# Kernel tuning notes

Hardware: AMD Instinct MI355X
Metric: run time of the kernel (lower is better)

Reference implementation:

```python
import jax, jax.numpy as jnp
import numpy as np


def gcn_conv(x, src, dst, W, b, num_nodes):
    # PyG GCNConv with add_self_loops=True, symmetric normalization.
    # src/dst already include self-loops.
    ones = jnp.ones(src.shape[0], dtype=x.dtype)
    deg = jax.ops.segment_sum(ones, dst, num_segments=num_nodes)  # [N]
    dinv = jnp.where(deg > 0, jax.lax.rsqrt(deg), 0.0)
    norm = dinv[src] * dinv[dst]                                   # [E+N]
    h = x @ W                                                      # [N, out]
    msg = h[src] * norm[:, None]                                   # gather + scale
    out = jax.ops.segment_sum(msg, dst, num_segments=num_nodes)    # scatter-add
    return out + b


def setup_inputs() -> dict:
    key = jax.random.key(0)
    k1, k2, k3, k4 = jax.random.split(key, 4)
    N, E = 50000, 1600000
    IN, HID, OUT = 1536, 256, 128
    x = jax.random.normal(k1, (N, IN), dtype=jnp.float32)
    edge_index = jax.random.randint(k2, (2, E), 0, N, dtype=jnp.int64)
    # Glorot-style scaled weights
    W1 = jax.random.normal(k3, (IN, HID), dtype=jnp.float32) / np.sqrt(IN)
    W2 = jax.random.normal(k4, (HID, OUT), dtype=jnp.float32) / np.sqrt(HID)
    b1 = jnp.zeros((HID,), dtype=jnp.float32)
    b2 = jnp.zeros((OUT,), dtype=jnp.float32)
    return {"x": x, "edge_index": edge_index, "W1": W1, "b1": b1,
            "W2": W2, "b2": b2, "num_nodes": N}


def reference(x, edge_index, W1, b1, W2, b2, num_nodes):
    loop = jnp.arange(num_nodes, dtype=edge_index.dtype)
    src = jnp.concatenate([edge_index[0], loop])
    dst = jnp.concatenate([edge_index[1], loop])
    h = gcn_conv(x, src, dst, W1, b1, num_nodes)
    h = jax.nn.relu(h)
    h = gcn_conv(h, src, dst, W2, b2, num_nodes)
    # F.normalize(h, dim=1): x / max(||x||_2, 1e-12)
    nrm = jnp.linalg.norm(h, axis=1, keepdims=True)
    return h / jnp.maximum(nrm, 1e-12)
```

## Files before the change

kernel.cpp:

```cpp
#include <hip/hip_runtime.h>

typedef __attribute__((ext_vector_type(4))) float f32x4;
typedef __attribute__((ext_vector_type(2))) float f32x2;
typedef __attribute__((ext_vector_type(8))) short s16x8;

static __device__ __forceinline__ unsigned short f2bf(float f) {
  unsigned int u = __builtin_bit_cast(unsigned int, f);
  u += 0x7fffu + ((u >> 16) & 1u);
  return (unsigned short)(u >> 16);
}
static __device__ __forceinline__ float bf2f(unsigned short h) {
  unsigned int u = ((unsigned int)h) << 16;
  return __builtin_bit_cast(float, u);
}

static __device__ __forceinline__ void gload_lds16(const void* g, void* l) {
  __builtin_amdgcn_global_load_lds(
      (const __attribute__((address_space(1))) unsigned int*)g,
      (__attribute__((address_space(3))) unsigned int*)l, 16, 0, 0);
}

__global__ void zero_k(int* p, int n) {
  int i = blockIdx.x * 256 + threadIdx.x;
  if (i < n) p[i] = 0;
}
__global__ void deg_count_k(const int* __restrict__ edges, int* cnt, int E) {
  int e = blockIdx.x * 256 + threadIdx.x;
  if (e < E) atomicAdd(&cnt[edges[E + e]], 1);
}

__global__ __launch_bounds__(256) void scan1_k(const int* __restrict__ cnt,
                                               int* __restrict__ loc,
                                               int* __restrict__ bsum, int N) {
  int t = threadIdx.x;
  int i0 = blockIdx.x * 1024 + t * 4;
  int c[4];
#pragma unroll
  for (int j = 0; j < 4; ++j) c[j] = (i0 + j < N) ? cnt[i0 + j] : 0;
  int tsum = c[0] + c[1] + c[2] + c[3];
  int lane = t & 63, wv = t >> 6;
  int incl = tsum;
#pragma unroll
  for (int off = 1; off < 64; off <<= 1) {
    int u = __shfl_up(incl, off, 64);
    if (lane >= off) incl += u;
  }
  __shared__ int ws[4];
  if (lane == 63) ws[wv] = incl;
  __syncthreads();
  int wbase = 0;
  for (int w = 0; w < wv; ++w) wbase += ws[w];
  int run = wbase + incl - tsum;
#pragma unroll
  for (int j = 0; j < 4; ++j) {
    if (i0 + j < N) loc[i0 + j] = run;
    run += c[j];
  }
  if (t == 255) bsum[blockIdx.x] = wbase + incl;
}
__global__ void scan2_k(int* bsum, int nb) {
  int lane = threadIdx.x;
  int v = (lane < nb) ? bsum[lane] : 0;
  int incl = v;
#pragma unroll
  for (int off = 1; off < 64; off <<= 1) {
    int u = __shfl_up(incl, off, 64);
    if (lane >= off) incl += u;
  }
  if (lane < nb) bsum[lane] = incl - v;
}
__global__ void addoff_k(int* loc, int* cursor, const int* __restrict__ bsum,
                         const int* __restrict__ cnt, float* __restrict__ dinv, int N) {
  int i = blockIdx.x * 256 + threadIdx.x;
  if (i < N) {
    int v = loc[i] + bsum[i >> 10];
    loc[i] = v;
    cursor[i] = v;
    dinv[i] = rsqrtf((float)(cnt[i] + 1));
  }
}
__global__ void fill_k(const int* __restrict__ edges, int* cursor,
                       int* __restrict__ csr, int E) {
  int e = blockIdx.x * 256 + threadIdx.x;
  if (e < E) {
    int s = edges[e], d = edges[E + e];
    int pos = atomicAdd(&cursor[d], 1);
    csr[pos] = s;
  }
}

__global__ __launch_bounds__(256) void convw_k(const float* __restrict__ W,
                                               unsigned short* __restrict__ Wt,
                                               int K, int Nn) {
  __shared__ float t[32][33];
  const int tx = threadIdx.x & 31, ty = threadIdx.x >> 5;
  const int k0 = blockIdx.x * 32, n0 = blockIdx.y * 32;
#pragma unroll
  for (int r = 0; r < 32; r += 8)
    t[r + ty][tx] = W[(long long)(k0 + r + ty) * Nn + (n0 + tx)];
  __syncthreads();
#pragma unroll
  for (int r = 0; r < 32; r += 8)
    Wt[(long long)(n0 + r + ty) * K + (k0 + tx)] = f2bf(t[tx][r + ty]);
}

template <int KTOT, int NTOT, int BM, bool A_BF16>
__global__ __launch_bounds__(256, 3) void gemm_k(
    const void* __restrict__ Aptr, const unsigned short* __restrict__ Bt,
    const float* __restrict__ dinv, unsigned short* __restrict__ outg, int M) {
  constexpr int BK = 32;
  constexpr int LDA = BK + 8;
  constexpr int MI = BM / 16;
  constexpr int STRIP = NTOT / 4;
  constexpr int NF = STRIP / 16;
  constexpr int BCH = (NTOT / 16) / 4;
  constexpr int ACH = (BM / 16) / 4;
  constexpr int NT = KTOT / BK;
  constexpr int TPR = 256 / BM;
  constexpr int FPT = BK / TPR;

  __shared__ unsigned short Asm_[2][BM * LDA];
  __shared__ unsigned short Bsm_[2][NTOT * BK];

  const int tid = threadIdx.x;
  const int wave = tid >> 6;
  const int lane = tid & 63;
  const int fr = lane & 15;
  const int quad = lane >> 4;
  const int m0 = blockIdx.x * BM;

  f32x4 acc[MI][NF];
#pragma unroll
  for (int i = 0; i < MI; ++i)
#pragma unroll
    for (int j = 0; j < NF; ++j) { f32x4 z = {0.f, 0.f, 0.f, 0.f}; acc[i][j] = z; }

  const int sl_r = lane >> 2;
  const int sl_s = (lane & 3) ^ ((lane >> 3) & 3);

  auto stageB = [&](int k0, int buf) {
#pragma unroll
    for (int c = 0; c < BCH; ++c) {
      int cc = wave * BCH + c;
      int r = cc * 16 + sl_r;
      const unsigned short* gp = Bt + (long long)r * KTOT + k0 + sl_s * 8;
      gload_lds16(gp, &Bsm_[buf][cc * 512]);
    }
  };
  auto stageA_h = [&](int k0, int buf) {
    const unsigned short* Ah = (const unsigned short*)Aptr;
#pragma unroll
    for (int c = 0; c < ACH; ++c) {
      int cc = wave * ACH + c;
      int r = cc * 16 + sl_r;
      const unsigned short* gp = Ah + (long long)(m0 + r) * KTOT + k0 + sl_s * 8;
      gload_lds16(gp, &Asm_[buf][cc * 512]);
    }
  };

  const int sr = tid / TPR;
  const int sc = (tid % TPR) * FPT;
  const bool arow_ok = (m0 + sr) < M;
  const float* arowf = (const float*)Aptr + (long long)(m0 + sr) * KTOT;
  float va[FPT];
  auto loadA = [&](int k0) {
    if (arow_ok) {
#pragma unroll
      for (int c = 0; c < FPT / 4; ++c) {
        f32x4 v = *(const f32x4*)(arowf + k0 + sc + c * 4);
#pragma unroll
        for (int j = 0; j < 4; ++j) va[c * 4 + j] = v[j];
      }
    } else {
#pragma unroll
      for (int j = 0; j < FPT; ++j) va[j] = 0.0f;
    }
  };
  auto cvtWriteA = [&](int buf) {
#pragma unroll
    for (int c = 0; c < FPT / 8; ++c) {
      s16x8 h;
#pragma unroll
      for (int j = 0; j < 8; ++j) h[j] = (short)f2bf(va[c * 8 + j]);
      *(s16x8*)&Asm_[buf][sr * LDA + sc + c * 8] = h;
    }
  };

  stageB(0, 0);
  if constexpr (A_BF16) {
    stageA_h(0, 0);
  } else {
    loadA(0);
    cvtWriteA(0);
    if (NT > 1) loadA(BK);
  }

  const int xsl = (fr >> 1) & 3;
  for (int kt = 0; kt < NT; ++kt) {
    const int cur = kt & 1;
    __syncthreads();
    if (kt + 1 < NT) {
      stageB((kt + 1) * BK, cur ^ 1);
      if constexpr (A_BF16) {
        stageA_h((kt + 1) * BK, cur ^ 1);
      } else {
        cvtWriteA(cur ^ 1);
        if (kt + 2 < NT) loadA((kt + 2) * BK);
      }
    }

    s16x8 af[MI], bfr[NF];
#pragma unroll
    for (int mi = 0; mi < MI; ++mi) {
      if constexpr (A_BF16)
        af[mi] = *(const s16x8*)&Asm_[cur][(mi * 16 + fr) * BK + ((quad ^ xsl) << 3)];
      else
        af[mi] = *(const s16x8*)&Asm_[cur][(mi * 16 + fr) * LDA + quad * 8];
    }
#pragma unroll
    for (int ni = 0; ni < NF; ++ni)
      bfr[ni] = *(const s16x8*)&Bsm_[cur][(wave * STRIP + ni * 16 + fr) * BK + ((quad ^ xsl) << 3)];
#pragma unroll
    for (int mi = 0; mi < MI; ++mi)
#pragma unroll
      for (int ni = 0; ni < NF; ++ni)
        acc[mi][ni] = __builtin_amdgcn_mfma_f32_16x16x32_bf16(af[mi], bfr[ni], acc[mi][ni], 0, 0, 0);
  }

#pragma unroll
  for (int mi = 0; mi < MI; ++mi) {
    int mbase = mi * 16 + quad * 4;
#pragma unroll
    for (int r = 0; r < 4; ++r) {
      int gm = m0 + mbase + r;
      if (gm < M) {
        float dv = dinv[gm];
#pragma unroll
        for (int ni = 0; ni < NF; ++ni) {
          int col = wave * STRIP + ni * 16 + fr;
          outg[(long long)gm * NTOT + col] = f2bf(acc[mi][ni][r] * dv);
        }
      }
    }
  }
}

__global__ __launch_bounds__(256) void agg1_k(const int* __restrict__ csr,
                                              const int* __restrict__ row,
                                              const int* __restrict__ cnt,
                                              const unsigned short* __restrict__ g,
                                              const float* __restrict__ bias,
                                              const float* __restrict__ dinv,
                                              unsigned short* __restrict__ h, int N) {
  const int wave = threadIdx.x >> 6, lane = threadIdx.x & 63;
  const int node = blockIdx.x * 4 + wave;
  if (node >= N) return;
  const int grp = lane >> 5, sub = lane & 31;
  const int f0 = sub * 8;
  float s[8];
#pragma unroll
  for (int k = 0; k < 8; ++k) s[k] = 0.0f;
  const int start = row[node], len = cnt[node];
  int j = 0;
  for (; j + 8 <= len; j += 8) {
    int idx[4];
#pragma unroll
    for (int t = 0; t < 4; ++t) idx[t] = csr[start + j + t * 2 + grp];
    s16x8 v[4];
#pragma unroll
    for (int t = 0; t < 4; ++t) v[t] = *(const s16x8*)&g[(long long)idx[t] * 256 + f0];
#pragma unroll
    for (int t = 0; t < 4; ++t)
#pragma unroll
      for (int k = 0; k < 8; ++k) s[k] += bf2f((unsigned short)v[t][k]);
  }
  for (; j < len; j += 2) {
    int jt = j + grp;
    bool val = jt < len;
    int idx = csr[start + (val ? jt : 0)];
    s16x8 v = *(const s16x8*)&g[(long long)idx * 256 + f0];
    float m = val ? 1.0f : 0.0f;
#pragma unroll
    for (int k = 0; k < 8; ++k) s[k] += m * bf2f((unsigned short)v[k]);
  }
#pragma unroll
  for (int k = 0; k < 8; ++k) s[k] += __shfl_xor(s[k], 32, 64);
  s16x8 sv = *(const s16x8*)&g[(long long)node * 256 + f0];
#pragma unroll
  for (int k = 0; k < 8; ++k) s[k] += bf2f((unsigned short)sv[k]);
  const float dv = dinv[node];
  f32x4 b0 = *(const f32x4*)&bias[f0];
  f32x4 b1v = *(const f32x4*)&bias[f0 + 4];
  if (grp == 0) {
    s16x8 o;
#pragma unroll
    for (int k = 0; k < 4; ++k) o[k] = (short)f2bf(fmaxf(0.0f, b0[k] + dv * s[k]));
#pragma unroll
    for (int k = 0; k < 4; ++k) o[4 + k] = (short)f2bf(fmaxf(0.0f, b1v[k] + dv * s[4 + k]));
    *(s16x8*)&h[(long long)node * 256 + f0] = o;
  }
}

__global__ __launch_bounds__(256) void agg2_k(const int* __restrict__ csr,
                                              const int* __restrict__ row,
                                              const int* __restrict__ cnt,
                                              const unsigned short* __restrict__ g,
                                              const float* __restrict__ b2,
                                              const float* __restrict__ dinv,
                                              float* __restrict__ out, int N) {
  const int wave = threadIdx.x >> 6, lane = threadIdx.x & 63;
  const int node = blockIdx.x * 4 + wave;
  if (node >= N) return;
  const int grp = lane >> 4, sub = lane & 15;
  const int f0 = sub * 8;
  float s[8];
#pragma unroll
  for (int k = 0; k < 8; ++k) s[k] = 0.0f;
  const int start = row[node], len = cnt[node];
  int j = 0;
  for (; j + 8 <= len; j += 8) {
    int idx[2];
#pragma unroll
    for (int t = 0; t < 2; ++t) idx[t] = csr[start + j + t * 4 + grp];
    s16x8 v[2];
#pragma unroll
    for (int t = 0; t < 2; ++t) v[t] = *(const s16x8*)&g[(long long)idx[t] * 128 + f0];
#pragma unroll
    for (int t = 0; t < 2; ++t)
#pragma unroll
      for (int k = 0; k < 8; ++k) s[k] += bf2f((unsigned short)v[t][k]);
  }
  for (; j < len; j += 4) {
    int jt = j + grp;
    bool val = jt < len;
    int idx = csr[start + (val ? jt : 0)];
    s16x8 v = *(const s16x8*)&g[(long long)idx * 128 + f0];
    float m = val ? 1.0f : 0.0f;
#pragma unroll
    for (int k = 0; k < 8; ++k) s[k] += m * bf2f((unsigned short)v[k]);
  }
#pragma unroll
  for (int k = 0; k < 8; ++k) s[k] += __shfl_xor(s[k], 16, 64);
#pragma unroll
  for (int k = 0; k < 8; ++k) s[k] += __shfl_xor(s[k], 32, 64);
  s16x8 sv = *(const s16x8*)&g[(long long)node * 128 + f0];
#pragma unroll
  for (int k = 0; k < 8; ++k) s[k] += bf2f((unsigned short)sv[k]);
  const float dv = dinv[node];
  f32x4 b0 = *(const f32x4*)&b2[f0];
  f32x4 b1v = *(const f32x4*)&b2[f0 + 4];
  float x[8];
#pragma unroll
  for (int k = 0; k < 4; ++k) x[k] = b0[k] + dv * s[k];
#pragma unroll
  for (int k = 0; k < 4; ++k) x[4 + k] = b1v[k] + dv * s[4 + k];
  float ss = 0.0f;
#pragma unroll
  for (int k = 0; k < 8; ++k) ss += x[k] * x[k];
#pragma unroll
  for (int off = 1; off < 16; off <<= 1) ss += __shfl_xor(ss, off, 64);
  const float inv = 1.0f / fmaxf(sqrtf(ss), 1e-12f);
  if (grp == 0) {
    f32x4 o0 = {x[0] * inv, x[1] * inv, x[2] * inv, x[3] * inv};
    f32x4 o1 = {x[4] * inv, x[5] * inv, x[6] * inv, x[7] * inv};
    *(f32x4*)&out[(long long)node * 128 + f0] = o0;
    *(f32x4*)&out[(long long)node * 128 + f0 + 4] = o1;
  }
}

extern "C" void kernel_launch(void* const* d_in, const int* in_sizes, int n_in,
                              void* d_out, int out_size, void* d_ws, size_t ws_size,
                              hipStream_t stream) {
  const float* x = (const float*)d_in[0];
  const int* edges = (const int*)d_in[1];
  const float* W1 = (const float*)d_in[2];
  const float* b1 = (const float*)d_in[3];
  const float* W2 = (const float*)d_in[4];
  const float* b2 = (const float*)d_in[5];
  float* out = (float*)d_out;

  const int HID = in_sizes[3];
  const int OUT = in_sizes[5];
  const int IN = in_sizes[2] / HID;
  const int N = in_sizes[0] / IN;
  const int E = in_sizes[1] / 2;

  size_t off = 0;
  auto carve = [&](size_t bytes) {
    void* p = (char*)d_ws + off;
    off += (bytes + 255) & ~(size_t)255;
    return p;
  };
  int* cnt = (int*)carve((size_t)N * 4);
  int* cursor = (int*)carve((size_t)N * 4);
  int* row = (int*)carve((size_t)N * 4);
  int* bsum = (int*)carve(64 * 4);
  int* csr = (int*)carve((size_t)E * 4 + 1024);
  float* dinv = (float*)carve((size_t)N * 4);
  unsigned short* W1t = (unsigned short*)carve((size_t)IN * HID * 2);
  unsigned short* W2t = (unsigned short*)carve((size_t)HID * OUT * 2);
  unsigned short* g1 = (unsigned short*)carve((size_t)N * HID * 2);
  unsigned short* acc1 = (unsigned short*)carve((size_t)N * HID * 2);
  unsigned short* g2 = (unsigned short*)carve((size_t)N * OUT * 2);
  (void)ws_size; (void)n_in; (void)out_size;

  const int nb = (N + 1023) / 1024;

  zero_k<<<(N + 255) / 256, 256, 0, stream>>>(cnt, N);
  deg_count_k<<<(E + 255) / 256, 256, 0, stream>>>(edges, cnt, E);

  scan1_k<<<nb, 256, 0, stream>>>(cnt, row, bsum, N);
  scan2_k<<<1, 64, 0, stream>>>(bsum, nb);
  addoff_k<<<(N + 255) / 256, 256, 0, stream>>>(row, cursor, bsum, cnt, dinv, N);
  fill_k<<<(E + 255) / 256, 256, 0, stream>>>(edges, cursor, csr, E);

  convw_k<<<dim3(IN / 32, HID / 32), 256, 0, stream>>>(W1, W1t, IN, HID);
  convw_k<<<dim3(HID / 32, OUT / 32), 256, 0, stream>>>(W2, W2t, HID, OUT);

  constexpr int BM = 64;
  int mtiles = (N + BM - 1) / BM;
  gemm_k<1536, 256, BM, false><<<mtiles, 256, 0, stream>>>(x, W1t, dinv, g1, N);
  agg1_k<<<(N + 3) / 4, 256, 0, stream>>>(csr, row, cnt, g1, b1, dinv, acc1, N);
  gemm_k<256, 128, BM, true><<<mtiles, 256, 0, stream>>>(acc1, W2t, dinv, g2, N);
  agg2_k<<<(N + 3) / 4, 256, 0, stream>>>(csr, row, cnt, g2, b2, dinv, out, N);
}
```

Before: 866.7 us.

## Deepen GEMM pipeline to triple-buffered LDS with 128-row tiles and register prefetch

Reworks the GEMM main loop into a three-stage LDS ring with a three-deep register prefetch of fp32 A rows. Waits use explicit s_waitcnt vmcnt counts and raw s_barrier instead of __syncthreads. The M tile grows from 64 to 128 rows, and A loads become nontemporal with clamped row indices instead of bounds branches. The goal is to hide the global-load latency of the large x matrix and halve how often B is reloaded. The cost is more LDS and registers per block (launch bounds drop to 2 blocks per SM) and fragile hand-counted wait logic.

```diff
diff --git a/kernel.cpp b/kernel.cpp
--- a/kernel.cpp
+++ b/kernel.cpp
@@ -104,11 +104,11 @@
     Wt[(long long)(n0 + r + ty) * K + (k0 + tx)] = f2bf(t[tx][r + ty]);
 }
 
-template <int KTOT, int NTOT, int BM, bool A_BF16>
-__global__ __launch_bounds__(256, 3) void gemm_k(
+template <int KTOT, int NTOT, bool A_BF16>
+__global__ __launch_bounds__(256, 2) void gemm_k(
     const void* __restrict__ Aptr, const unsigned short* __restrict__ Bt,
     const float* __restrict__ dinv, unsigned short* __restrict__ outg, int M) {
-  constexpr int BK = 32;
+  constexpr int BM = 128, BK = 32;
   constexpr int LDA = BK + 8;
   constexpr int MI = BM / 16;
   constexpr int STRIP = NTOT / 4;
@@ -118,9 +118,11 @@
   constexpr int NT = KTOT / BK;
   constexpr int TPR = 256 / BM;
   constexpr int FPT = BK / TPR;
-
-  __shared__ unsigned short Asm_[2][BM * LDA];
-  __shared__ unsigned short Bsm_[2][NTOT * BK];
+  constexpr int ASZ = A_BF16 ? (BM * BK) : (BM * LDA);
+  constexpr int VM_N = A_BF16 ? 4 : 12;
+
+  __shared__ unsigned short Asm_[3][ASZ];
+  __shared__ unsigned short Bsm_[3][NTOT * BK];
 
   const int tid = threadIdx.x;
   const int wave = tid >> 6;
@@ -160,55 +162,31 @@
 
   const int sr = tid / TPR;
   const int sc = (tid % TPR) * FPT;
-  const bool arow_ok = (m0 + sr) < M;
-  const float* arowf = (const float*)Aptr + (long long)(m0 + sr) * KTOT;
-  float va[FPT];
-  auto loadA = [&](int k0) {
-    if (arow_ok) {
-#pragma unroll
-      for (int c = 0; c < FPT / 4; ++c) {
-        f32x4 v = *(const f32x4*)(arowf + k0 + sc + c * 4);
-#pragma unroll
-        for (int j = 0; j < 4; ++j) va[c * 4 + j] = v[j];
-      }
-    } else {
-#pragma unroll
-      for (int j = 0; j < FPT; ++j) va[j] = 0.0f;
-    }
-  };
-  auto cvtWriteA = [&](int buf) {
-#pragma unroll
-    for (int c = 0; c < FPT / 8; ++c) {
-      s16x8 h;
-#pragma unroll
-      for (int j = 0; j < 8; ++j) h[j] = (short)f2bf(va[c * 8 + j]);
-      *(s16x8*)&Asm_[buf][sr * LDA + sc + c * 8] = h;
-    }
-  };
-
-  stageB(0, 0);
-  if constexpr (A_BF16) {
-    stageA_h(0, 0);
-  } else {
-    loadA(0);
-    cvtWriteA(0);
-    if (NT > 1) loadA(BK);
-  }
+  const int arow = min(m0 + sr, M - 1);
+  const float* arowf = (const float*)Aptr + (long long)arow * KTOT;
+  float va0[FPT], va1[FPT], va2[FPT];
+
+#define LOADA(VA, K0)                                                          \
+  do {                                                                         \
+    _Pragma("unroll") for (int c = 0; c < FPT / 4; ++c) {                      \
+      f32x4 v = __builtin_nontemporal_load(                                    \
+          (const f32x4*)(arowf + (K0) + sc + c * 4));                          \
+      _Pragma("unroll") for (int j = 0; j < 4; ++j) VA[c * 4 + j] = v[j];      \
+    }                                                                          \
+  } while (0)
+
+#define CVTWA(VA, BUF)                                                         \
+  do {                                                                         \
+    _Pragma("unroll") for (int c = 0; c < FPT / 8; ++c) {                      \
+      s16x8 hh;                                                                \
+      _Pragma("unroll") for (int j = 0; j < 8; ++j)                            \
+          hh[j] = (short)f2bf(VA[c * 8 + j]);                                  \
+      *(s16x8*)&Asm_[BUF][sr * LDA + sc + c * 8] = hh;                         \
+    }                                                                          \
+  } while (0)
 
   const int xsl = (fr >> 1) & 3;
-  for (int kt = 0; kt < NT; ++kt) {
-    const int cur = kt & 1;
-    __syncthreads();
-    if (kt + 1 < NT) {
-      stageB((kt + 1) * BK, cur ^ 1);
-      if constexpr (A_BF16) {
-        stageA_h((kt + 1) * BK, cur ^ 1);
-      } else {
-        cvtWriteA(cur ^ 1);
-        if (kt + 2 < NT) loadA((kt + 2) * BK);
-      }
-    }
-
+  auto compute = [&](int cur) {
     s16x8 af[MI], bfr[NF];
 #pragma unroll
     for (int mi = 0; mi < MI; ++mi) {
@@ -225,7 +203,58 @@
 #pragma unroll
       for (int ni = 0; ni < NF; ++ni)
         acc[mi][ni] = __builtin_amdgcn_mfma_f32_16x16x32_bf16(af[mi], bfr[ni], acc[mi][ni], 0, 0, 0);
-  }
+  };
+
+  if constexpr (A_BF16) {
+    stageB(0, 0); stageA_h(0, 0);
+    stageB(BK, 1); stageA_h(BK, 1);
+  } else {
+    {
+      float vt[FPT];
+      LOADA(vt, 0);  CVTWA(vt, 0);
+      LOADA(vt, BK); CVTWA(vt, 1);
+    }
+    stageB(0, 0);
+    stageB(BK, 1);
+    __builtin_amdgcn_sched_barrier(0);
+    LOADA(va0, 2 * BK);
+    LOADA(va1, 3 * BK);
+    LOADA(va2, 4 * BK);
+  }
+
+#define GITER(J, P, PS, VA)                                                    \
+  {                                                                            \
+    if constexpr (VM_N == 12)                                                  \
+      asm volatile("s_waitcnt vmcnt(12) lgkmcnt(0)" ::: "memory");             \
+    else                                                                       \
+      asm volatile("s_waitcnt vmcnt(4) lgkmcnt(0)" ::: "memory");              \
+    __builtin_amdgcn_s_barrier();                                              \
+    __builtin_amdgcn_sched_barrier(0);                                         \
+    int ks_ = ((J) + 2 < NT) ? ((J) + 2) * BK : (KTOT - BK);                   \
+    stageB(ks_, (PS));                                                         \
+    if constexpr (A_BF16) {                                                    \
+      stageA_h(ks_, (PS));                                                     \
+    } else {                                                                   \
+      __builtin_amdgcn_sched_barrier(0);   \
+      CVTWA(VA, (PS));                                                         \
+      int kl_ = ((J) + 5 < NT) ? ((J) + 5) * BK : (KTOT - BK);                 \
+      LOADA(VA, kl_);                                                          \
+    }                                                                          \
+    compute(P);                                                                \
+  }
+
+  int j = 0;
+  for (; j + 3 <= NT; j += 3) {
+    GITER(j, 0, 2, va0);
+    GITER(j + 1, 1, 0, va1);
+    GITER(j + 2, 2, 1, va2);
+  }
+  if constexpr (NT % 3 >= 1) GITER(j, 0, 2, va0);
+  if constexpr (NT % 3 == 2) GITER(j + 1, 1, 0, va1);
+
+#undef GITER
+#undef LOADA
+#undef CVTWA
 
 #pragma unroll
   for (int mi = 0; mi < MI; ++mi) {
@@ -417,10 +446,9 @@
   convw_k<<<dim3(IN / 32, HID / 32), 256, 0, stream>>>(W1, W1t, IN, HID);
   convw_k<<<dim3(HID / 32, OUT / 32), 256, 0, stream>>>(W2, W2t, HID, OUT);
 
-  constexpr int BM = 64;
-  int mtiles = (N + BM - 1) / BM;
-  gemm_k<1536, 256, BM, false><<<mtiles, 256, 0, stream>>>(x, W1t, dinv, g1, N);
+  int mtiles = (N + 127) / 128;
+  gemm_k<1536, 256, false><<<mtiles, 256, 0, stream>>>(x, W1t, dinv, g1, N);
   agg1_k<<<(N + 3) / 4, 256, 0, stream>>>(csr, row, cnt, g1, b1, dinv, acc1, N);
-  gemm_k<256, 128, BM, true><<<mtiles, 256, 0, stream>>>(acc1, W2t, dinv, g2, N);
+  gemm_k<256, 128, true><<<mtiles, 256, 0, stream>>>(acc1, W2t, dinv, g2, N);
   agg2_k<<<(N + 3) / 4, 256, 0, stream>>>(csr, row, cnt, g2, b2, dinv, out, N);
 }
```

Result: slower. 891.8 us (+2.9%).

## Drop LDS staging in GEMM; load MFMA fragments directly from global memory

Applied to the files above, without the earlier changes.

Rewrites the GEMM kernel so each wave loads its A rows and B columns straight from global memory into MFMA register fragments, double-buffered in registers, with no LDS tiles and no block barriers. Blocks grow to 512 threads covering 128 rows, and each wave owns 32 rows and half of the output columns. A is read with nontemporal loads and converted to bf16 in registers. This removes LDS traffic and synchronisation, but B is now re-read from global or L2 by every wave, and the per-lane 16-byte loads are less coalesced.

```diff
diff --git a/kernel.cpp b/kernel.cpp
--- a/kernel.cpp
+++ b/kernel.cpp
@@ -12,12 +12,6 @@
 static __device__ __forceinline__ float bf2f(unsigned short h) {
   unsigned int u = ((unsigned int)h) << 16;
   return __builtin_bit_cast(float, u);
-}
-
-static __device__ __forceinline__ void gload_lds16(const void* g, void* l) {
-  __builtin_amdgcn_global_load_lds(
-      (const __attribute__((address_space(1))) unsigned int*)g,
-      (__attribute__((address_space(3))) unsigned int*)l, 16, 0, 0);
 }
 
 __global__ void zero_k(int* p, int n) {
@@ -104,30 +98,30 @@
     Wt[(long long)(n0 + r + ty) * K + (k0 + tx)] = f2bf(t[tx][r + ty]);
 }
 
-template <int KTOT, int NTOT, int BM, bool A_BF16>
-__global__ __launch_bounds__(256, 3) void gemm_k(
+template <int KTOT, int NTOT, bool A_BF16>
+__global__ __launch_bounds__(512, 2) void gemm_k(
     const void* __restrict__ Aptr, const unsigned short* __restrict__ Bt,
     const float* __restrict__ dinv, unsigned short* __restrict__ outg, int M) {
   constexpr int BK = 32;
-  constexpr int LDA = BK + 8;
-  constexpr int MI = BM / 16;
-  constexpr int STRIP = NTOT / 4;
+  constexpr int NT = KTOT / BK;
+  constexpr int STRIP = NTOT / 2;
   constexpr int NF = STRIP / 16;
-  constexpr int BCH = (NTOT / 16) / 4;
-  constexpr int ACH = (BM / 16) / 4;
-  constexpr int NT = KTOT / BK;
-  constexpr int TPR = 256 / BM;
-  constexpr int FPT = BK / TPR;
-
-  __shared__ unsigned short Asm_[2][BM * LDA];
-  __shared__ unsigned short Bsm_[2][NTOT * BK];
+  constexpr int MI = 2;
 
   const int tid = threadIdx.x;
   const int wave = tid >> 6;
   const int lane = tid & 63;
   const int fr = lane & 15;
   const int quad = lane >> 4;
-  const int m0 = blockIdx.x * BM;
+  const int mq = wave >> 1;
+  const int nh = wave & 1;
+  const int m0 = blockIdx.x * 128 + mq * 32;
+
+  const float* Af = (const float*)Aptr;
+  const unsigned short* Ah = (const unsigned short*)Aptr;
+  long long ar0 = (long long)min(m0 + 0 * 16 + fr, M - 1) * KTOT;
+  long long ar1 = (long long)min(m0 + 1 * 16 + fr, M - 1) * KTOT;
+  const unsigned short* bbase = Bt + (long long)(nh * STRIP + fr) * KTOT;
 
   f32x4 acc[MI][NF];
 #pragma unroll
@@ -135,109 +129,81 @@
 #pragma unroll
     for (int j = 0; j < NF; ++j) { f32x4 z = {0.f, 0.f, 0.f, 0.f}; acc[i][j] = z; }
 
-  const int sl_r = lane >> 2;
-  const int sl_s = (lane & 3) ^ ((lane >> 3) & 3);
-
-  auto stageB = [&](int k0, int buf) {
-#pragma unroll
-    for (int c = 0; c < BCH; ++c) {
-      int cc = wave * BCH + c;
-      int r = cc * 16 + sl_r;
-      const unsigned short* gp = Bt + (long long)r * KTOT + k0 + sl_s * 8;
-      gload_lds16(gp, &Bsm_[buf][cc * 512]);
+  f32x4 vaA[MI][2], vaB[MI][2];
+  s16x8 ahA[MI], ahB[MI];
+  s16x8 bfA[NF], bfB[NF];
+
+#define LDA_(VA, AH, KT)                                                       \
+  do {                                                                         \
+    const int k0_ = (KT) * BK + quad * 8;                                      \
+    if constexpr (A_BF16) {                                                    \
+      AH[0] = __builtin_nontemporal_load((const s16x8*)(Ah + ar0 + k0_));      \
+      AH[1] = __builtin_nontemporal_load((const s16x8*)(Ah + ar1 + k0_));      \
+    } else {                                                                   \
+      VA[0][0] = __builtin_nontemporal_load((const f32x4*)(Af + ar0 + k0_));   \
+      VA[0][1] = __builtin_nontemporal_load((const f32x4*)(Af + ar0 + k0_ + 4));\
+      VA[1][0] = __builtin_nontemporal_load((const f32x4*)(Af + ar1 + k0_));   \
+      VA[1][1] = __builtin_nontemporal_load((const f32x4*)(Af + ar1 + k0_ + 4));\
+    }                                                                          \
+  } while (0)
+
+#define LDB_(BF, KT)                                                           \
+  do {                                                                         \
+    const int k0_ = (KT) * BK + quad * 8;                                      \
+    _Pragma("unroll") for (int ni = 0; ni < NF; ++ni)                          \
+        BF[ni] = *(const s16x8*)(bbase + (long long)ni * 16 * KTOT + k0_);     \
+  } while (0)
+
+#define MM_(VA, AH, BF)                                                        \
+  do {                                                                         \
+    s16x8 af_[MI];                                                             \
+    if constexpr (A_BF16) {                                                    \
+      af_[0] = AH[0]; af_[1] = AH[1];                                          \
+    } else {                                                                   \
+      _Pragma("unroll") for (int mi = 0; mi < MI; ++mi) {                      \
+        s16x8 h_;                                                              \
+        _Pragma("unroll") for (int j = 0; j < 4; ++j) {                        \
+          h_[j] = (short)f2bf(VA[mi][0][j]);                                   \
+          h_[4 + j] = (short)f2bf(VA[mi][1][j]);                               \
+        }                                                                      \
+        af_[mi] = h_;                                                          \
+      }                                                                        \
+    }                                                                          \
+    _Pragma("unroll") for (int mi = 0; mi < MI; ++mi)                          \
+      _Pragma("unroll") for (int ni = 0; ni < NF; ++ni)                        \
+          acc[mi][ni] = __builtin_amdgcn_mfma_f32_16x16x32_bf16(               \
+              af_[mi], BF[ni], acc[mi][ni], 0, 0, 0);                          \
+  } while (0)
+
+  LDA_(vaA, ahA, 0);
+  LDB_(bfA, 0);
+
+  for (int kp = 0; kp < NT / 2; ++kp) {
+    const int kt = 2 * kp;
+    LDA_(vaB, ahB, kt + 1);
+    LDB_(bfB, kt + 1);
+    MM_(vaA, ahA, bfA);
+    if (kt + 2 < NT) {
+      LDA_(vaA, ahA, kt + 2);
+      LDB_(bfA, kt + 2);
     }
-  };
-  auto stageA_h = [&](int k0, int buf) {
-    const unsigned short* Ah = (const unsigned short*)Aptr;
-#pragma unroll
-    for (int c = 0; c < ACH; ++c) {
-      int cc = wave * ACH + c;
-      int r = cc * 16 + sl_r;
-      const unsigned short* gp = Ah + (long long)(m0 + r) * KTOT + k0 + sl_s * 8;
-      gload_lds16(gp, &Asm_[buf][cc * 512]);
-    }
-  };
-
-  const int sr = tid / TPR;
-  const int sc = (tid % TPR) * FPT;
-  const bool arow_ok = (m0 + sr) < M;
-  const float* arowf = (const float*)Aptr + (long long)(m0 + sr) * KTOT;
-  float va[FPT];
-  auto loadA = [&](int k0) {
-    if (arow_ok) {
-#pragma unroll
-      for (int c = 0; c < FPT / 4; ++c) {
-        f32x4 v = *(const f32x4*)(arowf + k0 + sc + c * 4);
-#pragma unroll
-        for (int j = 0; j < 4; ++j) va[c * 4 + j] = v[j];
-      }
-    } else {
-#pragma unroll
-      for (int j = 0; j < FPT; ++j) va[j] = 0.0f;
-    }
-  };
-  auto cvtWriteA = [&](int buf) {
-#pragma unroll
-    for (int c = 0; c < FPT / 8; ++c) {
-      s16x8 h;
-#pragma unroll
-      for (int j = 0; j < 8; ++j) h[j] = (short)f2bf(va[c * 8 + j]);
-      *(s16x8*)&Asm_[buf][sr * LDA + sc + c * 8] = h;
-    }
-  };
-
-  stageB(0, 0);
-  if constexpr (A_BF16) {
-    stageA_h(0, 0);
-  } else {
-    loadA(0);
-    cvtWriteA(0);
-    if (NT > 1) loadA(BK);
-  }
-
-  const int xsl = (fr >> 1) & 3;
-  for (int kt = 0; kt < NT; ++kt) {
-    const int cur = kt & 1;
-    __syncthreads();
-    if (kt + 1 < NT) {
-      stageB((kt + 1) * BK, cur ^ 1);
-      if constexpr (A_BF16) {
-        stageA_h((kt + 1) * BK, cur ^ 1);
-      } else {
-        cvtWriteA(cur ^ 1);
-        if (kt + 2 < NT) loadA((kt + 2) * BK);
-      }
-    }
-
-    s16x8 af[MI], bfr[NF];
-#pragma unroll
-    for (int mi = 0; mi < MI; ++mi) {
-      if constexpr (A_BF16)
-        af[mi] = *(const s16x8*)&Asm_[cur][(mi * 16 + fr) * BK + ((quad ^ xsl) << 3)];
-      else
-        af[mi] = *(const s16x8*)&Asm_[cur][(mi * 16 + fr) * LDA + quad * 8];
-    }
-#pragma unroll
-    for (int ni = 0; ni < NF; ++ni)
-      bfr[ni] = *(const s16x8*)&Bsm_[cur][(wave * STRIP + ni * 16 + fr) * BK + ((quad ^ xsl) << 3)];
-#pragma unroll
-    for (int mi = 0; mi < MI; ++mi)
-#pragma unroll
-      for (int ni = 0; ni < NF; ++ni)
-        acc[mi][ni] = __builtin_amdgcn_mfma_f32_16x16x32_bf16(af[mi], bfr[ni], acc[mi][ni], 0, 0, 0);
-  }
+    MM_(vaB, ahB, bfB);
+  }
+#undef LDA_
+#undef LDB_
+#undef MM_
 
 #pragma unroll
   for (int mi = 0; mi < MI; ++mi) {
-    int mbase = mi * 16 + quad * 4;
+    int mbase = m0 + mi * 16 + quad * 4;
 #pragma unroll
     for (int r = 0; r < 4; ++r) {
-      int gm = m0 + mbase + r;
+      int gm = mbase + r;
       if (gm < M) {
         float dv = dinv[gm];
 #pragma unroll
         for (int ni = 0; ni < NF; ++ni) {
-          int col = wave * STRIP + ni * 16 + fr;
+          int col = nh * STRIP + ni * 16 + fr;
           outg[(long long)gm * NTOT + col] = f2bf(acc[mi][ni][r] * dv);
         }
       }
@@ -417,10 +383,9 @@
   convw_k<<<dim3(IN / 32, HID / 32), 256, 0, stream>>>(W1, W1t, IN, HID);
   convw_k<<<dim3(HID / 32, OUT / 32), 256, 0, stream>>>(W2, W2t, HID, OUT);
 
-  constexpr int BM = 64;
-  int mtiles = (N + BM - 1) / BM;
-  gemm_k<1536, 256, BM, false><<<mtiles, 256, 0, stream>>>(x, W1t, dinv, g1, N);
+  int mtiles = (N + 127) / 128;
+  gemm_k<1536, 256, false><<<mtiles, 512, 0, stream>>>(x, W1t, dinv, g1, N);
   agg1_k<<<(N + 3) / 4, 256, 0, stream>>>(csr, row, cnt, g1, b1, dinv, acc1, N);
-  gemm_k<256, 128, BM, true><<<mtiles, 256, 0, stream>>>(acc1, W2t, dinv, g2, N);
+  gemm_k<256, 128, true><<<mtiles, 512, 0, stream>>>(acc1, W2t, dinv, g2, N);
   agg2_k<<<(N + 3) / 4, 256, 0, stream>>>(csr, row, cnt, g2, b2, dinv, out, N);
 }
```

Result: slower. 1.048 ms (+20.9%).
